# Performance work log

Measured on AMD Instinct MI355X. Metric: run time of the kernel, lower is better.

The kernel has to match this reference:

```python
import jax, jax.numpy as jnp
import numpy as np

PI = float(np.pi)

def erp_xyz_coords(h, w):
    # matches calculate_erp_coord: pixel grid -> uv -> unit-sphere xyz
    yy, xx = jnp.meshgrid(jnp.linspace(0.0, h - 1.0, h), jnp.linspace(0.0, w - 1.0, w), indexing='ij')
    u = (xx - (w / 2.0 + 0.5)) / w * 2.0 * PI
    v = (yy - (h / 2.0 + 0.5)) / h * PI
    xyz = jnp.stack([jnp.cos(v) * jnp.sin(u), jnp.sin(v), jnp.cos(v) * jnp.cos(u)], axis=-1)
    return xyz.reshape(h * w, 3)  # (HW, 3)


def setup_inputs() -> dict:
    key = jax.random.key(0)
    ks = jax.random.split(key, 16)
    B, C, H, W = 1, 128, 16, 32
    Nkv = 1280
    s = 0.02
    inp = {
        'erp_feature': jax.random.normal(ks[0], (B, C, H, W), jnp.float32),
        'ico_feature': jax.random.normal(ks[1], (B, Nkv, C), jnp.float32),
        'ico_coord': jax.random.normal(ks[2], (B, Nkv, 3), jnp.float32),
        # SA branch params (torch Linear: y = x @ W.T + b, W is (out,in))
        'Wq_sa': jax.random.normal(ks[3], (C, C), jnp.float32) * s,
        'Wkv_sa': jax.random.normal(ks[4], (2 * C, C), jnp.float32) * s,
        'proj_sa_w': jax.random.normal(ks[5], (C, C), jnp.float32) * s,
        'proj_sa_b': jnp.zeros((C,), jnp.float32),
        # DA branch params
        'Wq_da': jax.random.normal(ks[6], (C, C), jnp.float32) * s,
        'Wkv_da': jax.random.normal(ks[7], (2 * C, C), jnp.float32) * s,
        'Wdelta': jax.random.normal(ks[8], (C, 3), jnp.float32) * s,
        'proj_da_w': jax.random.normal(ks[9], (C, C), jnp.float32) * s,
        'proj_da_b': jnp.zeros((C,), jnp.float32),
        # gates
        'gate_sa_w': jax.random.normal(ks[10], (C, 2 * C), jnp.float32) * s,
        'gate_da_w': jax.random.normal(ks[11], (C, 2 * C), jnp.float32) * s,
    }
    return inp


def _forward(erp_feature, ico_feature, ico_coord,
             Wq_sa, Wkv_sa, proj_sa_w, proj_sa_b,
             Wq_da, Wkv_da, Wdelta, proj_da_w, proj_da_b,
             gate_sa_w, gate_da_w):
    B, C, H, W = erp_feature.shape
    Nq = H * W
    q = erp_feature.reshape(B, C, Nq).transpose(0, 2, 1)  # (B, Nq, C)
    qc = erp_xyz_coords(H, W)[None]                        # (1, Nq, 3) broadcasts over B

    # ---- SA branch (iteration = 1) ----
    q_sa = q @ Wq_sa.T                                     # (B, Nq, C)
    kv_sa = (ico_feature @ Wkv_sa.T).reshape(B, -1, 2, C)
    k_sa, v_sa = kv_sa[:, :, 0], kv_sa[:, :, 1]
    attn_sa = jax.nn.softmax(jnp.einsum('bqc,bkc->bqk', q_sa, k_sa) * (C ** -0.5), axis=-1)
    out_sa = jnp.einsum('bqk,bkc->bqc', attn_sa, v_sa)
    # faithful to torch: .transpose(1,2).reshape(B, Nq, C) scrambles layout
    out_sa = out_sa.transpose(0, 2, 1).reshape(B, Nq, C)
    sa = out_sa @ proj_sa_w.T + proj_sa_b

    # ---- DA branch (iteration = 1) ----
    q_da = q @ Wq_da.T
    kv_da = (ico_feature @ Wkv_da.T).reshape(B, -1, 2, C)
    k_da, v_da = kv_da[:, :, 0], kv_da[:, :, 1]
    # feature affinity: sum_c exp(-|q_c - k_c|)   -> (B, Nq, Nkv)
    feat_aff = jnp.exp(-jnp.abs(q_da[:, :, None, :] - k_da[:, None, :, :])).sum(-1)
    # positional term: (exp(-|dq - dk|) @ Wdelta.T).sum(-1) == exp(...) . Wdelta.sum(0)
    pos_exp = jnp.exp(-jnp.abs(qc[:, :, None, :] - ico_coord[:, None, :, :]))  # (B,Nq,Nkv,3)
    pos_aff = jnp.einsum('bqkt,t->bqk', pos_exp, Wdelta.sum(0))
    attn_da = jax.nn.softmax((feat_aff + pos_aff) * (1.0 / C), axis=-1)
    out_da = jnp.einsum('bqk,bkc->bqc', attn_da, v_da)
    da = out_da @ proj_da_w.T + proj_da_b

    # ---- gated fusion ----
    cat = jnp.concatenate([sa, da], axis=-1)               # (B, Nq, 2C)
    sa_factor = jax.nn.sigmoid(cat @ gate_sa_w.T)
    da_factor = jax.nn.sigmoid(cat @ gate_da_w.T)
    fused = sa_factor * sa + da_factor * da                # (B, Nq, C)
    return fused.reshape(B, H, W, C).transpose(0, 3, 1, 2)  # (B, C, H, W)


def reference(erp_feature, ico_feature, ico_coord,
              Wq_sa, Wkv_sa, proj_sa_w, proj_sa_b,
              Wq_da, Wkv_da, Wdelta, proj_da_w, proj_da_b,
              gate_sa_w, gate_da_w):
    return _forward(erp_feature, ico_feature, ico_coord,
                    Wq_sa, Wkv_sa, proj_sa_w, proj_sa_b,
                    Wq_da, Wkv_da, Wdelta, proj_da_w, proj_da_b,
                    gate_sa_w, gate_da_w)
```

## Files before the change

kernel.cpp:

```cpp
#include <hip/hip_runtime.h>
#include <math.h>

#define NQ   512
#define NKV  1280
#define CDIM 128
#define L2E  1.4426950408889634f

__device__ __forceinline__ float fexp2(float x) { return __builtin_amdgcn_exp2f(x); }

#define OFF_WDSUM 0
#define OFF_SUMS  16
#define OFF_QSA   1056
#define OFF_QDA   66592
#define OFF_KSAT  132128
#define OFF_VSA   295968
#define OFF_KDAT  459808
#define OFF_VDA   623648
#define OFF_OUT   787488

__global__ __launch_bounds__(256) void prep_kernel(
    const float* __restrict__ erp, const float* __restrict__ ico,
    const float* __restrict__ wq_sa, const float* __restrict__ wq_da,
    const float* __restrict__ wkv_sa, const float* __restrict__ wkv_da,
    const float* __restrict__ wdelta, float* __restrict__ ws)
{
  int bx = blockIdx.x, t = threadIdx.x;
  if (bx < 320) {
    __shared__ float x4[4 * CDIM];
    int k0 = bx * 4;
    for (int i = t; i < 512; i += 256) {
      int ky = i >> 7, j = i & 127;
      x4[j * 4 + ky] = ico[(k0 + ky) * CDIM + j];
    }
    __syncthreads();
    const float4* wsa4 = (const float4*)(wkv_sa + t * CDIM);
    const float4* wda4 = (const float4*)(wkv_da + t * CDIM);
    float as0=0,as1=0,as2=0,as3=0, ad0=0,ad1=0,ad2=0,ad3=0;
    #pragma unroll 4
    for (int j4 = 0; j4 < 32; ++j4) {
      float4 wsv = wsa4[j4];
      float4 wdv = wda4[j4];
      float4 x0 = *(const float4*)&x4[(j4 * 4 + 0) * 4];
      float4 x1 = *(const float4*)&x4[(j4 * 4 + 1) * 4];
      float4 x2 = *(const float4*)&x4[(j4 * 4 + 2) * 4];
      float4 x3 = *(const float4*)&x4[(j4 * 4 + 3) * 4];
      as0 = fmaf(wsv.x, x0.x, as0); as1 = fmaf(wsv.x, x0.y, as1);
      as2 = fmaf(wsv.x, x0.z, as2); as3 = fmaf(wsv.x, x0.w, as3);
      ad0 = fmaf(wdv.x, x0.x, ad0); ad1 = fmaf(wdv.x, x0.y, ad1);
      ad2 = fmaf(wdv.x, x0.z, ad2); ad3 = fmaf(wdv.x, x0.w, ad3);
      as0 = fmaf(wsv.y, x1.x, as0); as1 = fmaf(wsv.y, x1.y, as1);
      as2 = fmaf(wsv.y, x1.z, as2); as3 = fmaf(wsv.y, x1.w, as3);
      ad0 = fmaf(wdv.y, x1.x, ad0); ad1 = fmaf(wdv.y, x1.y, ad1);
      ad2 = fmaf(wdv.y, x1.z, ad2); ad3 = fmaf(wdv.y, x1.w, ad3);
      as0 = fmaf(wsv.z, x2.x, as0); as1 = fmaf(wsv.z, x2.y, as1);
      as2 = fmaf(wsv.z, x2.z, as2); as3 = fmaf(wsv.z, x2.w, as3);
      ad0 = fmaf(wdv.z, x2.x, ad0); ad1 = fmaf(wdv.z, x2.y, ad1);
      ad2 = fmaf(wdv.z, x2.z, ad2); ad3 = fmaf(wdv.z, x2.w, ad3);
      as0 = fmaf(wsv.w, x3.x, as0); as1 = fmaf(wsv.w, x3.y, as1);
      as2 = fmaf(wsv.w, x3.z, as2); as3 = fmaf(wsv.w, x3.w, as3);
      ad0 = fmaf(wdv.w, x3.x, ad0); ad1 = fmaf(wdv.w, x3.y, ad1);
      ad2 = fmaf(wdv.w, x3.z, ad2); ad3 = fmaf(wdv.w, x3.w, ad3);
    }
    if (t < 128) {
      *(float4*)(ws + OFF_KSAT + t * NKV + k0) = make_float4(as0, as1, as2, as3);
      *(float4*)(ws + OFF_KDAT + t * NKV + k0) =
          make_float4(ad0 * L2E, ad1 * L2E, ad2 * L2E, ad3 * L2E);
    } else {
      int c = t - 128;
      ws[OFF_VSA + (k0 + 0) * CDIM + c] = as0;
      ws[OFF_VSA + (k0 + 1) * CDIM + c] = as1;
      ws[OFF_VSA + (k0 + 2) * CDIM + c] = as2;
      ws[OFF_VSA + (k0 + 3) * CDIM + c] = as3;
      ws[OFF_VDA + (k0 + 0) * CDIM + c] = ad0;
      ws[OFF_VDA + (k0 + 1) * CDIM + c] = ad1;
      ws[OFF_VDA + (k0 + 2) * CDIM + c] = ad2;
      ws[OFF_VDA + (k0 + 3) * CDIM + c] = ad3;
    }
  } else if (bx < 448) {
    __shared__ float q4[4 * CDIM];
    int n0 = (bx - 320) * 4;
    for (int i = t; i < 512; i += 256)
      q4[i] = erp[(i >> 2) * NQ + n0 + (i & 3)];
    __syncthreads();
    const float* w = (t < 128) ? wq_sa : wq_da;
    int c = t & 127;
    const float4* w4 = (const float4*)(w + c * CDIM);
    float a0 = 0.f, a1 = 0.f, a2 = 0.f, a3 = 0.f;
    #pragma unroll 8
    for (int j4 = 0; j4 < 32; ++j4) {
      float4 wv = w4[j4];
      float4 q0 = *(const float4*)&q4[(j4 * 4 + 0) * 4];
      float4 q1 = *(const float4*)&q4[(j4 * 4 + 1) * 4];
      float4 q2 = *(const float4*)&q4[(j4 * 4 + 2) * 4];
      float4 q3 = *(const float4*)&q4[(j4 * 4 + 3) * 4];
      a0 = fmaf(wv.x, q0.x, a0); a1 = fmaf(wv.x, q0.y, a1);
      a2 = fmaf(wv.x, q0.z, a2); a3 = fmaf(wv.x, q0.w, a3);
      a0 = fmaf(wv.y, q1.x, a0); a1 = fmaf(wv.y, q1.y, a1);
      a2 = fmaf(wv.y, q1.z, a2); a3 = fmaf(wv.y, q1.w, a3);
      a0 = fmaf(wv.z, q2.x, a0); a1 = fmaf(wv.z, q2.y, a1);
      a2 = fmaf(wv.z, q2.z, a2); a3 = fmaf(wv.z, q2.w, a3);
      a0 = fmaf(wv.w, q3.x, a0); a1 = fmaf(wv.w, q3.y, a1);
      a2 = fmaf(wv.w, q3.z, a2); a3 = fmaf(wv.w, q3.w, a3);
    }
    float sc = (t < 128) ? 1.0f : L2E;
    float* o = ws + ((t < 128) ? OFF_QSA : OFF_QDA);
    o[(n0 + 0) * CDIM + c] = a0 * sc;
    o[(n0 + 1) * CDIM + c] = a1 * sc;
    o[(n0 + 2) * CDIM + c] = a2 * sc;
    o[(n0 + 3) * CDIM + c] = a3 * sc;
  } else if (bx == 448) {
    *(float4*)(ws + OFF_SUMS + t * 4) = make_float4(0.f, 0.f, 0.f, 0.f);
    if (t < 3) {
      float s = 0.f;
      for (int i = 0; i < 128; ++i) s += wdelta[i * 3 + t];
      ws[OFF_WDSUM + t] = s;
    }
  } else {
    int base = OFF_OUT + (bx - 449) * 1024 + t * 4;
    *(float4*)(ws + base) = make_float4(0.f, 0.f, 0.f, 0.f);
  }
}

__global__ __launch_bounds__(256) void attn_kernel(
    const float* __restrict__ coord, float* __restrict__ ws)
{
  __shared__ __align__(16) float qjf[128][4];
  __shared__ __align__(16) float se[4][256];
  __shared__ __align__(16) float kch[2][16][128];
  __shared__ float red[4][4];
  __shared__ float qcr[4][3];
  __shared__ float wdl[3];
  int b = blockIdx.x, t = threadIdx.x;
  int br = (b < 1280) ? 1 : 0;
  int n0, k0;
  if (br) { int g = b / 10;          n0 = g * 4; k0 = (b - g * 10) * 128; }
  else    { int bb = b - 1280, g = bb / 5; n0 = g * 4; k0 = (bb - g * 5) * 256; }

  const float* qsrc = ws + (br ? OFF_QDA : OFF_QSA);
  for (int i = t; i < 512; i += 256)
    qjf[i >> 2][i & 3] = qsrc[(n0 + (i & 3)) * CDIM + (i >> 2)];
  if (br) {
    if (t < 4) {
      int n = n0 + t;
      float x = (float)(n & 31), y = (float)(n >> 5);
      float u  = (x - 16.5f) * 0.19634954084936207f;
      float vv = (y -  8.5f) * 0.19634954084936207f;
      float cv = cosf(vv);
      qcr[t][0] = cv * sinf(u) * L2E;
      qcr[t][1] = sinf(vv) * L2E;
      qcr[t][2] = cv * cosf(u) * L2E;
    }
    if (t >= 64 && t < 67) wdl[t - 64] = ws[OFF_WDSUM + (t - 64)];
  }
  __syncthreads();

  if (br) {
    int kl = t & 127, rp = t >> 7;
    int k = k0 + kl, rp2 = rp * 2;
    float c0 = coord[3 * k]     * L2E;
    float c1 = coord[3 * k + 1] * L2E;
    float c2 = coord[3 * k + 2] * L2E;
    float w0 = wdl[0], w1 = wdl[1], w2 = wdl[2];
    float pA = w0 * fexp2(-fabsf(qcr[rp2][0] - c0))
             + w1 * fexp2(-fabsf(qcr[rp2][1] - c1))
             + w2 * fexp2(-fabsf(qcr[rp2][2] - c2));
    float pB = w0 * fexp2(-fabsf(qcr[rp2 + 1][0] - c0))
             + w1 * fexp2(-fabsf(qcr[rp2 + 1][1] - c1))
             + w2 * fexp2(-fabsf(qcr[rp2 + 1][2] - c2));
    const float* kbase = ws + OFF_KDAT + k0;
    int srow = t >> 5;
    int scol = (t & 31) * 4;
    *(float4*)&kch[0][srow][scol] =
        *(const float4*)(kbase + (srow) * NKV + scol);
    *(float4*)&kch[0][srow + 8][scol] =
        *(const float4*)(kbase + (srow + 8) * NKV + scol);
    __syncthreads();
    float accA = 0.f, accB = 0.f;
    int cur = 0;
    for (int jb = 0; jb < 128; jb += 16) {
      float4 nx0, nx1;
      bool more = (jb + 16) < 128;
      if (more) {
        nx0 = *(const float4*)(kbase + (jb + 16 + srow) * NKV + scol);
        nx1 = *(const float4*)(kbase + (jb + 24 + srow) * NKV + scol);
      }
      #pragma unroll
      for (int j2 = 0; j2 < 16; ++j2) {
        float kv = kch[cur][j2][kl];
        float2 q = *(const float2*)&qjf[jb + j2][rp2];
        accA += fexp2(-fabsf(q.x - kv));
        accB += fexp2(-fabsf(q.y - kv));
      }
      __syncthreads();
      if (more) {
        *(float4*)&kch[cur ^ 1][srow][scol]     = nx0;
        *(float4*)&kch[cur ^ 1][srow + 8][scol] = nx1;
      }
      __syncthreads();
      cur ^= 1;
    }
    const float lsc = 0.0078125f * L2E;
    float eA = fexp2((accA + pA) * lsc);
    float eB = fexp2((accB + pB) * lsc);
    se[rp2][kl]     = eA;
    se[rp2 + 1][kl] = eB;
    float sA = eA, sB = eB;
    #pragma unroll
    for (int o = 32; o > 0; o >>= 1) {
      sA += __shfl_down(sA, o, 64); sB += __shfl_down(sB, o, 64);
    }
    if ((t & 63) == 0) { int w = t >> 6; red[w][0] = sA; red[w][1] = sB; }
    __syncthreads();
    if (t < 4) {
      int base = 2 * (t >> 1);
      atomicAdd(ws + OFF_SUMS + 512 + n0 + t,
                red[base][t & 1] + red[base + 1][t & 1]);
    }
    int c = t & 127, h = t >> 7;
    int kb = h * 64;
    const float* vp = ws + OFF_VDA + (k0 + kb) * CDIM + c;
    float a0 = 0.f, a1 = 0.f, a2 = 0.f, a3 = 0.f;
    #pragma unroll 2
    for (int ko = 0; ko < 64; ko += 4) {
      int kk = kb + ko;
      float4 p0 = *(const float4*)&se[0][kk];
      float4 p1 = *(const float4*)&se[1][kk];
      float4 p2 = *(const float4*)&se[2][kk];
      float4 p3 = *(const float4*)&se[3][kk];
      float v0 = vp[(ko + 0) * CDIM];
      float v1 = vp[(ko + 1) * CDIM];
      float v2 = vp[(ko + 2) * CDIM];
      float v3 = vp[(ko + 3) * CDIM];
      a0 = fmaf(p0.x, v0, a0); a0 = fmaf(p0.y, v1, a0);
      a0 = fmaf(p0.z, v2, a0); a0 = fmaf(p0.w, v3, a0);
      a1 = fmaf(p1.x, v0, a1); a1 = fmaf(p1.y, v1, a1);
      a1 = fmaf(p1.z, v2, a1); a1 = fmaf(p1.w, v3, a1);
      a2 = fmaf(p2.x, v0, a2); a2 = fmaf(p2.y, v1, a2);
      a2 = fmaf(p2.z, v2, a2); a2 = fmaf(p2.w, v3, a2);
      a3 = fmaf(p3.x, v0, a3); a3 = fmaf(p3.y, v1, a3);
      a3 = fmaf(p3.z, v2, a3); a3 = fmaf(p3.w, v3, a3);
    }
    float* op = ws + OFF_OUT + NQ * CDIM + c;
    atomicAdd(op + (n0 + 0) * CDIM, a0);
    atomicAdd(op + (n0 + 1) * CDIM, a1);
    atomicAdd(op + (n0 + 2) * CDIM, a2);
    atomicAdd(op + (n0 + 3) * CDIM, a3);
  } else {
    const float* kt = ws + OFF_KSAT + k0 + t;
    float acc0 = 0.f, acc1 = 0.f, acc2 = 0.f, acc3 = 0.f;
    for (int j4 = 0; j4 < 128; j4 += 4) {
      float kv0 = kt[(j4 + 0) * NKV];
      float kv1 = kt[(j4 + 1) * NKV];
      float kv2 = kt[(j4 + 2) * NKV];
      float kv3 = kt[(j4 + 3) * NKV];
      float4 q0 = *(const float4*)qjf[j4 + 0];
      float4 q1 = *(const float4*)qjf[j4 + 1];
      float4 q2 = *(const float4*)qjf[j4 + 2];
      float4 q3 = *(const float4*)qjf[j4 + 3];
      acc0 = fmaf(q0.x, kv0, acc0); acc1 = fmaf(q0.y, kv0, acc1);
      acc2 = fmaf(q0.z, kv0, acc2); acc3 = fmaf(q0.w, kv0, acc3);
      acc0 = fmaf(q1.x, kv1, acc0); acc1 = fmaf(q1.y, kv1, acc1);
      acc2 = fmaf(q1.z, kv1, acc2); acc3 = fmaf(q1.w, kv1, acc3);
      acc0 = fmaf(q2.x, kv2, acc0); acc1 = fmaf(q2.y, kv2, acc1);
      acc2 = fmaf(q2.z, kv2, acc2); acc3 = fmaf(q2.w, kv2, acc3);
      acc0 = fmaf(q3.x, kv3, acc0); acc1 = fmaf(q3.y, kv3, acc1);
      acc2 = fmaf(q3.z, kv3, acc2); acc3 = fmaf(q3.w, kv3, acc3);
    }
    const float scl2 = 0.088388347648318447f * L2E;
    float e0 = fexp2(acc0 * scl2);
    float e1 = fexp2(acc1 * scl2);
    float e2 = fexp2(acc2 * scl2);
    float e3 = fexp2(acc3 * scl2);
    se[0][t] = e0; se[1][t] = e1; se[2][t] = e2; se[3][t] = e3;
    float s0 = e0, s1 = e1, s2 = e2, s3 = e3;
    #pragma unroll
    for (int o = 32; o > 0; o >>= 1) {
      s0 += __shfl_down(s0, o, 64); s1 += __shfl_down(s1, o, 64);
      s2 += __shfl_down(s2, o, 64); s3 += __shfl_down(s3, o, 64);
    }
    if ((t & 63) == 0) {
      int w = t >> 6;
      red[w][0] = s0; red[w][1] = s1; red[w][2] = s2; red[w][3] = s3;
    }
    __syncthreads();
    if (t < 4)
      atomicAdd(ws + OFF_SUMS + n0 + t,
                red[0][t] + red[1][t] + red[2][t] + red[3][t]);
    int c = t & 127, h = t >> 7;
    int kb = h * 128;
    const float* vp = ws + OFF_VSA + (k0 + kb) * CDIM + c;
    float a0 = 0.f, a1 = 0.f, a2 = 0.f, a3 = 0.f;
    #pragma unroll 2
    for (int ko = 0; ko < 128; ko += 4) {
      int kk = kb + ko;
      float4 p0 = *(const float4*)&se[0][kk];
      float4 p1 = *(const float4*)&se[1][kk];
      float4 p2 = *(const float4*)&se[2][kk];
      float4 p3 = *(const float4*)&se[3][kk];
      float v0 = vp[(ko + 0) * CDIM];
      float v1 = vp[(ko + 1) * CDIM];
      float v2 = vp[(ko + 2) * CDIM];
      float v3 = vp[(ko + 3) * CDIM];
      a0 = fmaf(p0.x, v0, a0); a0 = fmaf(p0.y, v1, a0);
      a0 = fmaf(p0.z, v2, a0); a0 = fmaf(p0.w, v3, a0);
      a1 = fmaf(p1.x, v0, a1); a1 = fmaf(p1.y, v1, a1);
      a1 = fmaf(p1.z, v2, a1); a1 = fmaf(p1.w, v3, a1);
      a2 = fmaf(p2.x, v0, a2); a2 = fmaf(p2.y, v1, a2);
      a2 = fmaf(p2.z, v2, a2); a2 = fmaf(p2.w, v3, a2);
      a3 = fmaf(p3.x, v0, a3); a3 = fmaf(p3.y, v1, a3);
      a3 = fmaf(p3.z, v2, a3); a3 = fmaf(p3.w, v3, a3);
    }
    float* op = ws + OFF_OUT + c;
    atomicAdd(op + (n0 + 0) * CDIM, a0);
    atomicAdd(op + (n0 + 1) * CDIM, a1);
    atomicAdd(op + (n0 + 2) * CDIM, a2);
    atomicAdd(op + (n0 + 3) * CDIM, a3);
  }
}

__global__ __launch_bounds__(256) void finalize_kernel(
    const float* __restrict__ psa, const float* __restrict__ bsa,
    const float* __restrict__ pda, const float* __restrict__ bda,
    const float* __restrict__ gsa, const float* __restrict__ gda,
    float* __restrict__ out, float* __restrict__ ws)
{
  __shared__ float sain[2][CDIM];
  __shared__ float dain[2][CDIM];
  __shared__ float cat[2][2 * CDIM];
  __shared__ float gl[2][2][CDIM];
  int i0 = blockIdx.x * 2, t = threadIdx.x;
  int h = t >> 7, c = t & 127;
  #pragma unroll
  for (int rr = 0; rr < 2; ++rr) {
    int i = i0 + rr;
    if (h == 0) {
      int row = (i & 3) * 128 + c;
      float s = ws[OFF_SUMS + row];
      sain[rr][c] = ws[OFF_OUT + row * CDIM + (i >> 2)] / s;
    } else {
      float s = ws[OFF_SUMS + 512 + i];
      dain[rr][c] = ws[OFF_OUT + NQ * CDIM + i * CDIM + c] / s;
    }
  }
  __syncthreads();
  {
    const float4* w4 = (const float4*)((h ? pda : psa) + c * CDIM);
    const float* in0 = h ? dain[0] : sain[0];
    const float* in1 = h ? dain[1] : sain[1];
    float a0 = 0, a1 = 0, b0 = 0, b1 = 0;
    #pragma unroll 8
    for (int j4 = 0; j4 < 32; ++j4) {
      float4 wv = w4[j4];
      float4 x0 = *(const float4*)&in0[j4 * 4];
      float4 x1 = *(const float4*)&in1[j4 * 4];
      a0 = fmaf(wv.x, x0.x, a0); a1 = fmaf(wv.y, x0.y, a1);
      a0 = fmaf(wv.z, x0.z, a0); a1 = fmaf(wv.w, x0.w, a1);
      b0 = fmaf(wv.x, x1.x, b0); b1 = fmaf(wv.y, x1.y, b1);
      b0 = fmaf(wv.z, x1.z, b0); b1 = fmaf(wv.w, x1.w, b1);
    }
    float bias = h ? bda[c] : bsa[c];
    cat[0][h * CDIM + c] = bias + a0 + a1;
    cat[1][h * CDIM + c] = bias + b0 + b1;
  }
  __syncthreads();
  {
    const float4* g4 = (const float4*)((h ? gda : gsa) + c * 2 * CDIM);
    float a0 = 0, a1 = 0, b0 = 0, b1 = 0;
    #pragma unroll 8
    for (int j4 = 0; j4 < 64; ++j4) {
      float4 gv = g4[j4];
      float4 c0 = *(const float4*)&cat[0][j4 * 4];
      float4 c1 = *(const float4*)&cat[1][j4 * 4];
      a0 = fmaf(gv.x, c0.x, a0); a1 = fmaf(gv.y, c0.y, a1);
      a0 = fmaf(gv.z, c0.z, a0); a1 = fmaf(gv.w, c0.w, a1);
      b0 = fmaf(gv.x, c1.x, b0); b1 = fmaf(gv.y, c1.y, b1);
      b0 = fmaf(gv.z, c1.z, b0); b1 = fmaf(gv.w, c1.w, b1);
    }
    gl[0][h][c] = 1.0f / (1.0f + __expf(-(a0 + a1)));
    gl[1][h][c] = 1.0f / (1.0f + __expf(-(b0 + b1)));
  }
  __syncthreads();
  {
    int i = i0 + h;
    out[c * NQ + i] = gl[h][0][c] * cat[h][c] + gl[h][1][c] * cat[h][CDIM + c];
  }
}

extern "C" void kernel_launch(void* const* d_in, const int* in_sizes, int n_in,
                              void* d_out, int out_size, void* d_ws, size_t ws_size,
                              hipStream_t stream)
{
  (void)in_sizes; (void)n_in; (void)out_size; (void)ws_size;
  const float* erp       = (const float*)d_in[0];
  const float* ico       = (const float*)d_in[1];
  const float* coord     = (const float*)d_in[2];
  const float* wq_sa     = (const float*)d_in[3];
  const float* wkv_sa    = (const float*)d_in[4];
  const float* proj_sa_w = (const float*)d_in[5];
  const float* proj_sa_b = (const float*)d_in[6];
  const float* wq_da     = (const float*)d_in[7];
  const float* wkv_da    = (const float*)d_in[8];
  const float* wdelta    = (const float*)d_in[9];
  const float* proj_da_w = (const float*)d_in[10];
  const float* proj_da_b = (const float*)d_in[11];
  const float* gate_sa   = (const float*)d_in[12];
  const float* gate_da   = (const float*)d_in[13];
  float* out = (float*)d_out;
  float* ws  = (float*)d_ws;

  hipLaunchKernelGGL(prep_kernel, dim3(577), dim3(256), 0, stream,
                     erp, ico, wq_sa, wq_da, wkv_sa, wkv_da, wdelta, ws);
  hipLaunchKernelGGL(attn_kernel, dim3(1920), dim3(256), 0, stream,
                     coord, ws);
  hipLaunchKernelGGL(finalize_kernel, dim3(256), dim3(256), 0, stream,
                     proj_sa_w, proj_sa_b, proj_da_w, proj_da_b,
                     gate_sa, gate_da, out, ws);
}
```

Measured before the change: 138.9 us.

## Unify SA and DA attention paths with shared LDS-staged K tiles

The SA branch now uses the same block shape as the DA branch: 128 keys per block and 2 queries per thread. K tiles are staged through double-buffered shared memory instead of strided global loads, which raises the grid from 1920 to 2560 blocks. The q tile layout is transposed so each thread reads float4 vectors along the channel axis, and the pipelined loop drops one barrier per iteration. The cost is more blocks and more atomic adds for the SA partial sums, plus a branch inside the shared inner loop.

```diff
diff --git a/kernel.cpp b/kernel.cpp
--- a/kernel.cpp
+++ b/kernel.cpp
@@ -124,21 +124,27 @@
 __global__ __launch_bounds__(256) void attn_kernel(
     const float* __restrict__ coord, float* __restrict__ ws)
 {
-  __shared__ __align__(16) float qjf[128][4];
-  __shared__ __align__(16) float se[4][256];
+  __shared__ __align__(16) float qjf[4][128];
+  __shared__ __align__(16) float se[4][128];
   __shared__ __align__(16) float kch[2][16][128];
-  __shared__ float red[4][4];
+  __shared__ float red[4][2];
   __shared__ float qcr[4][3];
   __shared__ float wdl[3];
   int b = blockIdx.x, t = threadIdx.x;
   int br = (b < 1280) ? 1 : 0;
-  int n0, k0;
-  if (br) { int g = b / 10;          n0 = g * 4; k0 = (b - g * 10) * 128; }
-  else    { int bb = b - 1280, g = bb / 5; n0 = g * 4; k0 = (bb - g * 5) * 256; }
+  int bb = br ? b : b - 1280;
+  int g = bb / 10, z = bb - g * 10;
+  int n0 = g * 4, k0 = z * 128;
 
   const float* qsrc = ws + (br ? OFF_QDA : OFF_QSA);
   for (int i = t; i < 512; i += 256)
-    qjf[i >> 2][i & 3] = qsrc[(n0 + (i & 3)) * CDIM + (i >> 2)];
+    qjf[i >> 7][i & 127] = qsrc[(n0 + (i >> 7)) * CDIM + (i & 127)];
+
+  int srow = t >> 5, scol = (t & 31) * 4;
+  const float* kbase = ws + (br ? OFF_KDAT : OFF_KSAT) + k0;
+  *(float4*)&kch[0][srow][scol]     = *(const float4*)(kbase + srow * NKV + scol);
+  *(float4*)&kch[0][srow + 8][scol] = *(const float4*)(kbase + (srow + 8) * NKV + scol);
+
   if (br) {
     if (t < 4) {
       int n = n0 + t;
@@ -154,168 +160,124 @@
   }
   __syncthreads();
 
+  int kl = t & 127, rp = t >> 7, rp2 = rp * 2;
+  int k = k0 + kl;
+
+  float pA = 0.f, pB = 0.f;
   if (br) {
-    int kl = t & 127, rp = t >> 7;
-    int k = k0 + kl, rp2 = rp * 2;
     float c0 = coord[3 * k]     * L2E;
     float c1 = coord[3 * k + 1] * L2E;
     float c2 = coord[3 * k + 2] * L2E;
     float w0 = wdl[0], w1 = wdl[1], w2 = wdl[2];
-    float pA = w0 * fexp2(-fabsf(qcr[rp2][0] - c0))
-             + w1 * fexp2(-fabsf(qcr[rp2][1] - c1))
-             + w2 * fexp2(-fabsf(qcr[rp2][2] - c2));
-    float pB = w0 * fexp2(-fabsf(qcr[rp2 + 1][0] - c0))
-             + w1 * fexp2(-fabsf(qcr[rp2 + 1][1] - c1))
-             + w2 * fexp2(-fabsf(qcr[rp2 + 1][2] - c2));
-    const float* kbase = ws + OFF_KDAT + k0;
-    int srow = t >> 5;
-    int scol = (t & 31) * 4;
-    *(float4*)&kch[0][srow][scol] =
-        *(const float4*)(kbase + (srow) * NKV + scol);
-    *(float4*)&kch[0][srow + 8][scol] =
-        *(const float4*)(kbase + (srow + 8) * NKV + scol);
-    __syncthreads();
-    float accA = 0.f, accB = 0.f;
-    int cur = 0;
-    for (int jb = 0; jb < 128; jb += 16) {
-      float4 nx0, nx1;
-      bool more = (jb + 16) < 128;
-      if (more) {
-        nx0 = *(const float4*)(kbase + (jb + 16 + srow) * NKV + scol);
-        nx1 = *(const float4*)(kbase + (jb + 24 + srow) * NKV + scol);
+    pA = w0 * fexp2(-fabsf(qcr[rp2][0] - c0))
+       + w1 * fexp2(-fabsf(qcr[rp2][1] - c1))
+       + w2 * fexp2(-fabsf(qcr[rp2][2] - c2));
+    pB = w0 * fexp2(-fabsf(qcr[rp2 + 1][0] - c0))
+       + w1 * fexp2(-fabsf(qcr[rp2 + 1][1] - c1))
+       + w2 * fexp2(-fabsf(qcr[rp2 + 1][2] - c2));
+  }
+
+  float accA = 0.f, accB = 0.f;
+  int cur = 0;
+  for (int jb = 0; jb < 128; jb += 16) {
+    float4 nx0, nx1;
+    bool more = (jb + 16) < 128;
+    if (more) {
+      nx0 = *(const float4*)(kbase + (jb + 16 + srow) * NKV + scol);
+      nx1 = *(const float4*)(kbase + (jb + 24 + srow) * NKV + scol);
+    }
+    if (br) {
+      #pragma unroll
+      for (int j4 = 0; j4 < 16; j4 += 4) {
+        float4 qA = *(const float4*)&qjf[rp2][jb + j4];
+        float4 qB = *(const float4*)&qjf[rp2 + 1][jb + j4];
+        float k0v = kch[cur][j4 + 0][kl];
+        float k1v = kch[cur][j4 + 1][kl];
+        float k2v = kch[cur][j4 + 2][kl];
+        float k3v = kch[cur][j4 + 3][kl];
+        accA += fexp2(-fabsf(qA.x - k0v)); accB += fexp2(-fabsf(qB.x - k0v));
+        accA += fexp2(-fabsf(qA.y - k1v)); accB += fexp2(-fabsf(qB.y - k1v));
+        accA += fexp2(-fabsf(qA.z - k2v)); accB += fexp2(-fabsf(qB.z - k2v));
+        accA += fexp2(-fabsf(qA.w - k3v)); accB += fexp2(-fabsf(qB.w - k3v));
       }
+    } else {
       #pragma unroll
-      for (int j2 = 0; j2 < 16; ++j2) {
-        float kv = kch[cur][j2][kl];
-        float2 q = *(const float2*)&qjf[jb + j2][rp2];
-        accA += fexp2(-fabsf(q.x - kv));
-        accB += fexp2(-fabsf(q.y - kv));
+      for (int j4 = 0; j4 < 16; j4 += 4) {
+        float4 qA = *(const float4*)&qjf[rp2][jb + j4];
+        float4 qB = *(const float4*)&qjf[rp2 + 1][jb + j4];
+        float k0v = kch[cur][j4 + 0][kl];
+        float k1v = kch[cur][j4 + 1][kl];
+        float k2v = kch[cur][j4 + 2][kl];
+        float k3v = kch[cur][j4 + 3][kl];
+        accA = fmaf(qA.x, k0v, accA); accB = fmaf(qB.x, k0v, accB);
+        accA = fmaf(qA.y, k1v, accA); accB = fmaf(qB.y, k1v, accB);
+        accA = fmaf(qA.z, k2v, accA); accB = fmaf(qB.z, k2v, accB);
+        accA = fmaf(qA.w, k3v, accA); accB = fmaf(qB.w, k3v, accB);
       }
+    }
+    if (more) {
+      *(float4*)&kch[cur ^ 1][srow][scol]     = nx0;
+      *(float4*)&kch[cur ^ 1][srow + 8][scol] = nx1;
       __syncthreads();
-      if (more) {
-        *(float4*)&kch[cur ^ 1][srow][scol]     = nx0;
-        *(float4*)&kch[cur ^ 1][srow + 8][scol] = nx1;
-      }
-      __syncthreads();
-      cur ^= 1;
-    }
+    }
+    cur ^= 1;
+  }
+
+  float eA, eB;
+  if (br) {
     const float lsc = 0.0078125f * L2E;
-    float eA = fexp2((accA + pA) * lsc);
-    float eB = fexp2((accB + pB) * lsc);
-    se[rp2][kl]     = eA;
-    se[rp2 + 1][kl] = eB;
-    float sA = eA, sB = eB;
-    #pragma unroll
-    for (int o = 32; o > 0; o >>= 1) {
-      sA += __shfl_down(sA, o, 64); sB += __shfl_down(sB, o, 64);
-    }
-    if ((t & 63) == 0) { int w = t >> 6; red[w][0] = sA; red[w][1] = sB; }
-    __syncthreads();
-    if (t < 4) {
-      int base = 2 * (t >> 1);
-      atomicAdd(ws + OFF_SUMS + 512 + n0 + t,
-                red[base][t & 1] + red[base + 1][t & 1]);
-    }
-    int c = t & 127, h = t >> 7;
-    int kb = h * 64;
-    const float* vp = ws + OFF_VDA + (k0 + kb) * CDIM + c;
-    float a0 = 0.f, a1 = 0.f, a2 = 0.f, a3 = 0.f;
-    #pragma unroll 2
-    for (int ko = 0; ko < 64; ko += 4) {
-      int kk = kb + ko;
-      float4 p0 = *(const float4*)&se[0][kk];
-      float4 p1 = *(const float4*)&se[1][kk];
-      float4 p2 = *(const float4*)&se[2][kk];
-      float4 p3 = *(const float4*)&se[3][kk];
-      float v0 = vp[(ko + 0) * CDIM];
-      float v1 = vp[(ko + 1) * CDIM];
-      float v2 = vp[(ko + 2) * CDIM];
-      float v3 = vp[(ko + 3) * CDIM];
-      a0 = fmaf(p0.x, v0, a0); a0 = fmaf(p0.y, v1, a0);
-      a0 = fmaf(p0.z, v2, a0); a0 = fmaf(p0.w, v3, a0);
-      a1 = fmaf(p1.x, v0, a1); a1 = fmaf(p1.y, v1, a1);
-      a1 = fmaf(p1.z, v2, a1); a1 = fmaf(p1.w, v3, a1);
-      a2 = fmaf(p2.x, v0, a2); a2 = fmaf(p2.y, v1, a2);
-      a2 = fmaf(p2.z, v2, a2); a2 = fmaf(p2.w, v3, a2);
-      a3 = fmaf(p3.x, v0, a3); a3 = fmaf(p3.y, v1, a3);
-      a3 = fmaf(p3.z, v2, a3); a3 = fmaf(p3.w, v3, a3);
-    }
-    float* op = ws + OFF_OUT + NQ * CDIM + c;
-    atomicAdd(op + (n0 + 0) * CDIM, a0);
-    atomicAdd(op + (n0 + 1) * CDIM, a1);
-    atomicAdd(op + (n0 + 2) * CDIM, a2);
-    atomicAdd(op + (n0 + 3) * CDIM, a3);
+    eA = fexp2((accA + pA) * lsc);
+    eB = fexp2((accB + pB) * lsc);
   } else {
-    const float* kt = ws + OFF_KSAT + k0 + t;
-    float acc0 = 0.f, acc1 = 0.f, acc2 = 0.f, acc3 = 0.f;
-    for (int j4 = 0; j4 < 128; j4 += 4) {
-      float kv0 = kt[(j4 + 0) * NKV];
-      float kv1 = kt[(j4 + 1) * NKV];
-      float kv2 = kt[(j4 + 2) * NKV];
-      float kv3 = kt[(j4 + 3) * NKV];
-      float4 q0 = *(const float4*)qjf[j4 + 0];
-      float4 q1 = *(const float4*)qjf[j4 + 1];
-      float4 q2 = *(const float4*)qjf[j4 + 2];
-      float4 q3 = *(const float4*)qjf[j4 + 3];
-      acc0 = fmaf(q0.x, kv0, acc0); acc1 = fmaf(q0.y, kv0, acc1);
-      acc2 = fmaf(q0.z, kv0, acc2); acc3 = fmaf(q0.w, kv0, acc3);
-      acc0 = fmaf(q1.x, kv1, acc0); acc1 = fmaf(q1.y, kv1, acc1);
-      acc2 = fmaf(q1.z, kv1, acc2); acc3 = fmaf(q1.w, kv1, acc3);
-      acc0 = fmaf(q2.x, kv2, acc0); acc1 = fmaf(q2.y, kv2, acc1);
-      acc2 = fmaf(q2.z, kv2, acc2); acc3 = fmaf(q2.w, kv2, acc3);
-      acc0 = fmaf(q3.x, kv3, acc0); acc1 = fmaf(q3.y, kv3, acc1);
-      acc2 = fmaf(q3.z, kv3, acc2); acc3 = fmaf(q3.w, kv3, acc3);
-    }
     const float scl2 = 0.088388347648318447f * L2E;
-    float e0 = fexp2(acc0 * scl2);
-    float e1 = fexp2(acc1 * scl2);
-    float e2 = fexp2(acc2 * scl2);
-    float e3 = fexp2(acc3 * scl2);
-    se[0][t] = e0; se[1][t] = e1; se[2][t] = e2; se[3][t] = e3;
-    float s0 = e0, s1 = e1, s2 = e2, s3 = e3;
-    #pragma unroll
-    for (int o = 32; o > 0; o >>= 1) {
-      s0 += __shfl_down(s0, o, 64); s1 += __shfl_down(s1, o, 64);
-      s2 += __shfl_down(s2, o, 64); s3 += __shfl_down(s3, o, 64);
-    }
-    if ((t & 63) == 0) {
-      int w = t >> 6;
-      red[w][0] = s0; red[w][1] = s1; red[w][2] = s2; red[w][3] = s3;
-    }
-    __syncthreads();
-    if (t < 4)
-      atomicAdd(ws + OFF_SUMS + n0 + t,
-                red[0][t] + red[1][t] + red[2][t] + red[3][t]);
-    int c = t & 127, h = t >> 7;
-    int kb = h * 128;
-    const float* vp = ws + OFF_VSA + (k0 + kb) * CDIM + c;
-    float a0 = 0.f, a1 = 0.f, a2 = 0.f, a3 = 0.f;
-    #pragma unroll 2
-    for (int ko = 0; ko < 128; ko += 4) {
-      int kk = kb + ko;
-      float4 p0 = *(const float4*)&se[0][kk];
-      float4 p1 = *(const float4*)&se[1][kk];
-      float4 p2 = *(const float4*)&se[2][kk];
-      float4 p3 = *(const float4*)&se[3][kk];
-      float v0 = vp[(ko + 0) * CDIM];
-      float v1 = vp[(ko + 1) * CDIM];
-      float v2 = vp[(ko + 2) * CDIM];
-      float v3 = vp[(ko + 3) * CDIM];
-      a0 = fmaf(p0.x, v0, a0); a0 = fmaf(p0.y, v1, a0);
-      a0 = fmaf(p0.z, v2, a0); a0 = fmaf(p0.w, v3, a0);
-      a1 = fmaf(p1.x, v0, a1); a1 = fmaf(p1.y, v1, a1);
-      a1 = fmaf(p1.z, v2, a1); a1 = fmaf(p1.w, v3, a1);
-      a2 = fmaf(p2.x, v0, a2); a2 = fmaf(p2.y, v1, a2);
-      a2 = fmaf(p2.z, v2, a2); a2 = fmaf(p2.w, v3, a2);
-      a3 = fmaf(p3.x, v0, a3); a3 = fmaf(p3.y, v1, a3);
-      a3 = fmaf(p3.z, v2, a3); a3 = fmaf(p3.w, v3, a3);
-    }
-    float* op = ws + OFF_OUT + c;
-    atomicAdd(op + (n0 + 0) * CDIM, a0);
-    atomicAdd(op + (n0 + 1) * CDIM, a1);
-    atomicAdd(op + (n0 + 2) * CDIM, a2);
-    atomicAdd(op + (n0 + 3) * CDIM, a3);
-  }
+    eA = fexp2(accA * scl2);
+    eB = fexp2(accB * scl2);
+  }
+  se[rp2][kl]     = eA;
+  se[rp2 + 1][kl] = eB;
+
+  float sA = eA, sB = eB;
+  #pragma unroll
+  for (int o = 32; o > 0; o >>= 1) {
+    sA += __shfl_down(sA, o, 64); sB += __shfl_down(sB, o, 64);
+  }
+  if ((t & 63) == 0) { int w = t >> 6; red[w][0] = sA; red[w][1] = sB; }
+  __syncthreads();
+  if (t < 4) {
+    int base = 2 * (t >> 1);
+    atomicAdd(ws + OFF_SUMS + br * 512 + n0 + t,
+              red[base][t & 1] + red[base + 1][t & 1]);
+  }
+
+  int c = t & 127, h = t >> 7;
+  int kb = h * 64;
+  const float* vp = ws + (br ? OFF_VDA : OFF_VSA) + (k0 + kb) * CDIM + c;
+  float a0 = 0.f, a1 = 0.f, a2 = 0.f, a3 = 0.f;
+  #pragma unroll 2
+  for (int ko = 0; ko < 64; ko += 4) {
+    int kk = kb + ko;
+    float4 p0 = *(const float4*)&se[0][kk];
+    float4 p1 = *(const float4*)&se[1][kk];
+    float4 p2 = *(const float4*)&se[2][kk];
+    float4 p3 = *(const float4*)&se[3][kk];
+    float v0 = vp[(ko + 0) * CDIM];
+    float v1 = vp[(ko + 1) * CDIM];
+    float v2 = vp[(ko + 2) * CDIM];
+    float v3 = vp[(ko + 3) * CDIM];
+    a0 = fmaf(p0.x, v0, a0); a0 = fmaf(p0.y, v1, a0);
+    a0 = fmaf(p0.z, v2, a0); a0 = fmaf(p0.w, v3, a0);
+    a1 = fmaf(p1.x, v0, a1); a1 = fmaf(p1.y, v1, a1);
+    a1 = fmaf(p1.z, v2, a1); a1 = fmaf(p1.w, v3, a1);
+    a2 = fmaf(p2.x, v0, a2); a2 = fmaf(p2.y, v1, a2);
+    a2 = fmaf(p2.z, v2, a2); a2 = fmaf(p2.w, v3, a2);
+    a3 = fmaf(p3.x, v0, a3); a3 = fmaf(p3.y, v1, a3);
+    a3 = fmaf(p3.z, v2, a3); a3 = fmaf(p3.w, v3, a3);
+  }
+  float* op = ws + OFF_OUT + br * (NQ * CDIM) + c;
+  atomicAdd(op + (n0 + 0) * CDIM, a0);
+  atomicAdd(op + (n0 + 1) * CDIM, a1);
+  atomicAdd(op + (n0 + 2) * CDIM, a2);
+  atomicAdd(op + (n0 + 3) * CDIM, a3);
 }
 
 __global__ __launch_bounds__(256) void finalize_kernel(
@@ -410,7 +372,7 @@
 
   hipLaunchKernelGGL(prep_kernel, dim3(577), dim3(256), 0, stream,
                      erp, ico, wq_sa, wq_da, wkv_sa, wkv_da, wdelta, ws);
-  hipLaunchKernelGGL(attn_kernel, dim3(1920), dim3(256), 0, stream,
+  hipLaunchKernelGGL(attn_kernel, dim3(2560), dim3(256), 0, stream,
                      coord, ws);
   hipLaunchKernelGGL(finalize_kernel, dim3(256), dim3(256), 0, stream,
                      proj_sa_w, proj_sa_b, proj_da_w, proj_da_b,
```

Result: slower. 142.3 us (+2.5%).
